# Kernel optimization log

Measured on AMD Instinct MI355X. Metric: run time of the kernel, lower is better.

Reference implementation:

```python
import jax, jax.numpy as jnp
import numpy as np

REPR_IN = (16, 16, 8)
REPR_OUT = (32, 16, 8)
NUM_BASIS = 16
MAX_RADIUS = 2.0
GAMMA = 16.0  # radial basis sharpness

def _dim(repr_):
    return sum(m * (2 * l + 1) for l, m in enumerate(repr_))

DIM_IN = _dim(REPR_IN)          # 104
SIZE_OUT = _dim(REPR_OUT)       # 120
NUM_GATES = sum(REPR_OUT[1:])   # 24
DIM_OUT = SIZE_OUT + NUM_GATES  # 144 (conv emits gates too)


def setup_inputs() -> dict:
    key = jax.random.key(0)
    k1, k2, k3, k4 = jax.random.split(key, 4)
    B, N, M = 4, 1024, 1024
    features = jax.random.normal(k1, (B, DIM_IN, M), jnp.float32)
    difference_matrix = jax.random.normal(k2, (B, N, M, 3), jnp.float32)
    relative_mask = jax.random.uniform(k3, (B, N, M), jnp.float32)
    W = jax.random.normal(k4, (NUM_BASIS, DIM_OUT, DIM_IN), jnp.float32) / np.sqrt(NUM_BASIS * DIM_IN)
    return {"features": features, "difference_matrix": difference_matrix,
            "relative_mask": relative_mask, "W": W}


def _radial_basis(diff):
    # diff: [B, N, M, 3] -> phi: [B, N, M, K]
    r = jnp.sqrt(jnp.sum(diff * diff, axis=-1) + 1e-12)
    centers = jnp.linspace(0.0, MAX_RADIUS, NUM_BASIS, dtype=diff.dtype)
    return jnp.exp(-GAMMA * jnp.square(r[..., None] - centers))


def reference(features, difference_matrix, relative_mask, W):
    # SE3PointConvolution: per-pair kernel K[b,n,m] = sum_k phi_k(|r_nm|) W[k]
    # masked by relative_mask; out[b,o,n] = sum_m K[b,n,m,o,i] feat[b,i,m].
    # Fused so the [B,N,M,144,104] kernel is never materialized.
    phi = _radial_basis(difference_matrix) * relative_mask[..., None]  # [B,N,M,K]
    tmp = jnp.einsum('bnmk,bim->bnki', phi, features)                  # [B,N,K,DIM_IN]
    y = jnp.einsum('bnki,koi->bon', tmp, W)                            # [B,DIM_OUT,N]

    B, _, N = y.shape
    # scalar (l=0) activation, bias=False
    outs = [jax.nn.relu(y[:, :REPR_OUT[0]])]
    # gates: last NUM_GATES channels, sigmoid
    g = jax.nn.sigmoid(y[:, SIZE_OUT:])
    begin_y, begin_g = REPR_OUT[0], 0
    for l, mul in enumerate(REPR_OUT):
        if l == 0 or mul == 0:
            continue
        d = 2 * l + 1
        fy = y[:, begin_y:begin_y + mul * d].reshape(B, mul, d, N)
        fg = g[:, begin_g:begin_g + mul].reshape(B, mul, 1, N)
        outs.append((fy * fg).reshape(B, mul * d, N))
        begin_y += mul * d
        begin_g += mul
    return jnp.concatenate(outs, axis=1)  # [B, SIZE_OUT, N]
```

## Files before the change

kernel.cpp:

```cpp
#include <hip/hip_runtime.h>


typedef __attribute__((ext_vector_type(4))) float f32x4;
typedef __attribute__((ext_vector_type(8))) short s16x8;

#define DI 104
#define DO 144
#define TTST 1688
#define YST 9

#define W_ELEMS 239616
#define F_ELEMS 425984

#define OFF_PHI0 0
#define OFF_PHI1 16384
#define OFF_FEAT0 32768
#define OFF_FEAT1 47104
#define OFF_Y 61440
#define SMEM_TOTAL (61440 + 144*9*4)

__device__ __forceinline__ float fexp2(float x) {
#if __has_builtin(__builtin_amdgcn_exp2f)
    return __builtin_amdgcn_exp2f(x);
#else
    return exp2f(x);
#endif
}
__device__ __forceinline__ float flog2(float x) {
#if __has_builtin(__builtin_amdgcn_logf)
    return __builtin_amdgcn_logf(x);
#else
    return log2f(x);
#endif
}
__device__ __forceinline__ float fsqrt_(float x) {
#if __has_builtin(__builtin_amdgcn_sqrtf)
    return __builtin_amdgcn_sqrtf(x);
#else
    return sqrtf(x);
#endif
}
__device__ __forceinline__ float frcp_(float x) {
#if __has_builtin(__builtin_amdgcn_rcpf)
    return __builtin_amdgcn_rcpf(x);
#else
    return 1.0f / x;
#endif
}
__device__ __forceinline__ unsigned int pkbf(float lo, float hi) {
    unsigned int a = __builtin_bit_cast(unsigned int, lo) + 0x8000u;
    unsigned int b = __builtin_bit_cast(unsigned int, hi) + 0x8000u;
    return __builtin_amdgcn_perm(b, a, 0x07060302u);
}
__device__ __forceinline__ unsigned short f2b(float f) {
    return (unsigned short)((__builtin_bit_cast(unsigned int, f) + 0x8000u) >> 16);
}

__global__ __launch_bounds__(256, 8)
void cvt_kernel(const float* __restrict__ feat_g, const float* __restrict__ W_g,
                unsigned short* __restrict__ ws)
{
    int gid = blockIdx.x * 256 + threadIdx.x;
    const float* src;
    unsigned short* dst;
    if (gid < W_ELEMS/8) {
        src = W_g + gid*8;  dst = ws + gid*8;
    } else {
        int g2 = gid - W_ELEMS/8;
        src = feat_g + g2*8; dst = ws + W_ELEMS + g2*8;
    }
    f32x4 a = *(const f32x4*)src;
    f32x4 b = *(const f32x4*)(src + 4);
    unsigned int o[4] = { pkbf(a[0],a[1]), pkbf(a[2],a[3]), pkbf(b[0],b[1]), pkbf(b[2],b[3]) };
    *(f32x4*)dst = *(f32x4*)o;
}

#define LOAD_DM(M0)                                                    \
    do {                                                               \
        const float* dp_ = diff_g + (dmrow + (M0) + pml)*3;            \
        dx0 = dp_[0]; dy0 = dp_[1]; dz0 = dp_[2];                      \
        dx1 = dp_[3]; dy1 = dp_[4]; dz1 = dp_[5];                      \
        const float* mp_ = mask_g + dmrow + (M0) + pml;                \
        mk0 = mp_[0]; mk1 = mp_[1];                                    \
    } while (0)

#define LOAD_FEAT(M0)                                                          \
    do {                                                                       \
        fr0 = *(const s16x8*)(featbf + fbase + ((size_t)fi0 << 10) + (M0) + (fj << 3)); \
        if (t < 320)                                                           \
            fr1 = *(const s16x8*)(featbf + fbase + ((size_t)fi1 << 10) + (M0) + (fj << 3)); \
    } while (0)

#define PHI_ANCHOR()                                                   \
    do {                                                               \
        float r0_ = fsqrt_(fmaf(dx0,dx0, fmaf(dy0,dy0, fmaf(dz0,dz0, 1e-12f)))); \
        float r1_ = fsqrt_(fmaf(dx1,dx1, fmaf(dy1,dy1, fmaf(dz1,dz1, 1e-12f)))); \
        float t0_ = r0_ - K0OFF, t1_ = r1_ - K0OFF;                    \
        va0 = fexp2(fmaf(CEXP*t0_, t0_, flog2(mk0)));                  \
        va1 = fexp2(fmaf(CEXP*t1_, t1_, flog2(mk1)));                  \
        wa0 = fexp2(fmaf(A1, r0_, S0B));                               \
        wa1 = fexp2(fmaf(A1, r1_, S0B));                               \
        float p0_ = wa0*wa0, p1_ = wa1*wa1;                            \
        float q0_ = fminf(p0_*p0_, 3.0e38f);                           \
        float q1_ = fminf(p1_*p1_, 3.0e38f);                           \
        vb0 = va0 * q0_ * U2_6;                                        \
        vb1 = va1 * q1_ * U2_6;                                        \
        wb0 = wa0 * U2_4;                                              \
        wb1 = wa1 * U2_4;                                              \
    } while (0)

#define PHI_WRITE_Q(BUF, V0, V1, W0, W1, J0)                           \
    do {                                                               \
        unsigned short* pw_ = (BUF) + phirow;                          \
        _Pragma("unroll")                                              \
        for (int j_ = 0; j_ < 4; ++j_) {                               \
            *(unsigned int*)(pw_ + ((J0) + j_)*64 + ((pblk ^ ((J0) + j_)) << 3)) = pkbf(V0, V1); \
            V0 *= W0; W0 *= U2;                                        \
            V1 *= W1; W1 *= U2;                                        \
        }                                                              \
    } while (0)

#define WRITE_FEAT(BUF)                                                \
    do {                                                               \
        *(s16x8*)((BUF) + fi0*64 + fjs) = fr0;                         \
        if (t < 320) *(s16x8*)((BUF) + fi1*64 + fjs) = fr1;            \
    } while (0)

#define GEMM1_HALF(PBUF, FBUF, KK)                                     \
    do {                                                               \
        const int mo_ = (((KK)*4 + q) ^ sw) << 3;                      \
        s16x8 a0_ = *(const s16x8*)((PBUF) + ((2*wr    )*16 + l15)*64 + mo_); \
        s16x8 a1_ = *(const s16x8*)((PBUF) + ((2*wr + 1)*16 + l15)*64 + mo_); \
        _Pragma("unroll")                                              \
        for (int cc_ = 0; cc_ < 4; ++cc_) {                            \
            if (ct0 + cc_ < 7) {                                       \
                s16x8 bf_ = *(const s16x8*)((FBUF) + ((ct0+cc_)*16 + l15)*64 + mo_); \
                acc[0][cc_] = __builtin_amdgcn_mfma_f32_16x16x32_bf16(a0_, bf_, acc[0][cc_], 0, 0, 0); \
                acc[1][cc_] = __builtin_amdgcn_mfma_f32_16x16x32_bf16(a1_, bf_, acc[1][cc_], 0, 0, 0); \
            }                                                          \
        }                                                              \
    } while (0)

__global__ __launch_bounds__(512, 4)
void pgb_kernel(const unsigned short* __restrict__ ws,
                const float* __restrict__ diff_g,
                const float* __restrict__ mask_g,
                float* __restrict__ out_g)
{
    const unsigned short* Wbf    = ws;
    const unsigned short* featbf = ws + W_ELEMS;

    __shared__ __align__(16) unsigned char smem[SMEM_TOTAL];
    unsigned short* Tt   = (unsigned short*)smem;
    float*          ylds = (float*)(smem + OFF_Y);
    unsigned short* phi0b  = (unsigned short*)(smem + OFF_PHI0);
    unsigned short* phi1b  = (unsigned short*)(smem + OFF_PHI1);
    unsigned short* feat0b = (unsigned short*)(smem + OFF_FEAT0);
    unsigned short* feat1b = (unsigned short*)(smem + OFF_FEAT1);

    const int t    = threadIdx.x;
    const int b    = blockIdx.x >> 7;
    const int n0   = (blockIdx.x & 127) << 3;
    const int wave = t >> 6;
    const int lane = t & 63;
    const int l15  = lane & 15;
    const int q    = lane >> 4;
    const int wr   = wave >> 1;
    const int ct0  = (wave & 1) << 2;
    const int sw   = l15 & 7;

    if (t < 256) {
        ((unsigned int*)(smem + OFF_FEAT0 + DI*128))[t] = 0u;
        ((unsigned int*)(smem + OFF_FEAT1 + DI*128))[t] = 0u;
    }

    f32x4 acc[2][4];
#pragma unroll
    for (int rr = 0; rr < 2; ++rr)
#pragma unroll
        for (int cc = 0; cc < 4; ++cc)
            acc[rr][cc] = (f32x4){0.f, 0.f, 0.f, 0.f};

    const int pn   = t >> 6;
    const int kh   = (t >> 5) & 1;
    const int pml  = (t & 31) << 1;
    const int pblk = (t & 31) >> 2;
    const int phirow = (pn*16 + kh*8)*64 + (pml & 7);
    const float CEXP = -23.083120654223414f;
    const float A1   = 6.155498841126244f;
    const float V2   = -0.8207331788168325f;
    const float U2   = fexp2(V2);
    const float U2_2 = U2*U2;
    const float U2_4 = U2_2*U2_2;
    const float U2_6 = U2_4*U2_2;
    const float K0OFF = kh ? 1.0666666666666667f : 0.f;
    const float S0B   = kh ? -6.976232019943076f : -0.41036658940841624f;
    const size_t dmrow = (size_t)((b << 10) + n0 + pn) << 10;

    const int fi0 = t >> 3, fj = t & 7;
    const int fi1 = 64 + (t >> 3);
    const int fjs = (fj ^ (fi0 & 7)) << 3;
    const size_t fbase = (size_t)b * DI << 10;

    float dx0, dy0, dz0, dx1, dy1, dz1, mk0, mk1;
    s16x8 fr0 = {}, fr1 = {};
    float va0, va1, wa0, wa1, vb0, vb1, wb0, wb1;

    LOAD_DM(0);
    LOAD_FEAT(0);
    PHI_ANCHOR();
    PHI_WRITE_Q(phi0b, va0, va1, wa0, wa1, 0);
    PHI_WRITE_Q(phi0b, vb0, vb1, wb0, wb1, 4);
    WRITE_FEAT(feat0b);
    LOAD_DM(64);
    LOAD_FEAT(64);

    for (int s = 0; s < 15; ++s) {
        unsigned short* rp = (s & 1) ? phi1b  : phi0b;
        unsigned short* rf = (s & 1) ? feat1b : feat0b;
        unsigned short* wp = (s & 1) ? phi0b  : phi1b;
        unsigned short* wf = (s & 1) ? feat0b : feat1b;
        __syncthreads();
        WRITE_FEAT(wf);
        PHI_ANCHOR();
        GEMM1_HALF(rp, rf, 0);
        PHI_WRITE_Q(wp, va0, va1, wa0, wa1, 0);
        GEMM1_HALF(rp, rf, 1);
        PHI_WRITE_Q(wp, vb0, vb1, wb0, wb1, 4);
        {
            const int mnext = (s < 14 ? (s + 2) : 15) * 64;
            LOAD_DM(mnext);
            LOAD_FEAT(mnext);
        }
    }
    __syncthreads();
    GEMM1_HALF(phi1b, feat1b, 0);
    GEMM1_HALF(phi1b, feat1b, 1);

    __syncthreads();

#pragma unroll
    for (int rr = 0; rr < 2; ++rr) {
        int nloc = 2*wr + rr;
#pragma unroll
        for (int cc = 0; cc < 4; ++cc) {
            int i = (ct0+cc)*16 + l15;
            if (ct0 + cc < 7 && i < DI) {
#pragma unroll
                for (int r = 0; r < 4; ++r)
                    Tt[nloc*TTST + (q*4+r)*DI + i] = f2b(acc[rr][cc][r]);
            }
        }
    }
    __syncthreads();

    f32x4 y0 = (f32x4){0.f,0.f,0.f,0.f}, y1 = (f32x4){0.f,0.f,0.f,0.f};
    const int o0 = wave*16 + l15;
    const int o1 = 128 + l15;
#pragma unroll 4
    for (int s3 = 0; s3 < 52; ++s3) {
        int a = s3*4 + q;
        int k = a / 13;
        int i = (a - k*13) << 3;
        s16x8 bf = *(const s16x8*)(Tt + (l15 & 7)*TTST + s3*32 + q*8);
        s16x8 af = *(const s16x8*)(Wbf + (size_t)(k*DO + o0)*DI + i);
        y0 = __builtin_amdgcn_mfma_f32_16x16x32_bf16(af, bf, y0, 0, 0, 0);
        if (wave == 0) {
            s16x8 ag = *(const s16x8*)(Wbf + (size_t)(k*DO + o1)*DI + i);
            y1 = __builtin_amdgcn_mfma_f32_16x16x32_bf16(ag, bf, y1, 0, 0, 0);
        }
    }
    if (l15 < 8) {
#pragma unroll
        for (int r = 0; r < 4; ++r)
            ylds[(wave*16 + q*4 + r)*YST + l15] = y0[r];
        if (wave == 0) {
#pragma unroll
            for (int r = 0; r < 4; ++r)
                ylds[(128 + q*4 + r)*YST + l15] = y1[r];
        }
    }
    __syncthreads();

    const float L2E = 1.4426950408889634f;
    for (int idx = t; idx < 120*8; idx += 512) {
        int o = idx >> 3, nn = idx & 7;
        float y = ylds[o*YST + nn];
        float v;
        if (o < 32) {
            v = fmaxf(y, 0.f);
        } else if (o < 80) {
            float g = ylds[(120 + (o-32)/3)*YST + nn];
            v = y * frcp_(1.f + fexp2(-g*L2E));
        } else {
            float g = ylds[(136 + (o-80)/5)*YST + nn];
            v = y * frcp_(1.f + fexp2(-g*L2E));
        }
        out_g[((size_t)(b*120 + o) << 10) + n0 + nn] = v;
    }
}

extern "C" void kernel_launch(void* const* d_in, const int* in_sizes, int n_in,
                              void* d_out, int out_size, void* d_ws, size_t ws_size,
                              hipStream_t stream) {
    const float* feat = (const float*)d_in[0];
    const float* diff = (const float*)d_in[1];
    const float* mask = (const float*)d_in[2];
    const float* W    = (const float*)d_in[3];
    float* out = (float*)d_out;
    unsigned short* ws = (unsigned short*)d_ws;
    (void)in_sizes; (void)n_in; (void)out_size; (void)ws_size;
    cvt_kernel<<<dim3((W_ELEMS + F_ELEMS)/8/256), dim3(256), 0, stream>>>(feat, W, ws);
    pgb_kernel<<<dim3(512), dim3(512), 0, stream>>>(ws, diff, mask, out);
}
```

Measured before the change: 141.4 us.

## Prepack W into MFMA-fragment order and add sched_group_barrier interleaving

```diff
diff --git a/kernel.cpp b/kernel.cpp
--- a/kernel.cpp
+++ b/kernel.cpp
@@ -11,6 +11,7 @@
 
 #define W_ELEMS 239616
 #define F_ELEMS 425984
+#define WP_BLKS 29952
 
 #define OFF_PHI0 0
 #define OFF_PHI1 16384
@@ -18,6 +19,8 @@
 #define OFF_FEAT1 47104
 #define OFF_Y 61440
 #define SMEM_TOTAL (61440 + 144*9*4)
+
+#define SGB(m, n) __builtin_amdgcn_sched_group_barrier((m), (n), 0)
 
 __device__ __forceinline__ float fexp2(float x) {
 #if __has_builtin(__builtin_amdgcn_exp2f)
@@ -63,11 +66,17 @@
     int gid = blockIdx.x * 256 + threadIdx.x;
     const float* src;
     unsigned short* dst;
-    if (gid < W_ELEMS/8) {
-        src = W_g + gid*8;  dst = ws + gid*8;
+    if (gid < WP_BLKS) {
+        int a = gid / 144;
+        int o = gid - a * 144;
+        int k = a / 13;
+        int im = (a - k * 13) << 3;
+        src = W_g + ((k * DO + o) * DI + im);
+        dst = ws + gid * 8;
     } else {
-        int g2 = gid - W_ELEMS/8;
-        src = feat_g + g2*8; dst = ws + W_ELEMS + g2*8;
+        int g2 = gid - WP_BLKS;
+        src = feat_g + g2 * 8;
+        dst = ws + W_ELEMS + g2 * 8;
     }
     f32x4 a = *(const f32x4*)src;
     f32x4 b = *(const f32x4*)(src + 4);
@@ -147,7 +156,7 @@
                 const float* __restrict__ mask_g,
                 float* __restrict__ out_g)
 {
-    const unsigned short* Wbf    = ws;
+    const unsigned short* Wp     = ws;
     const unsigned short* featbf = ws + W_ELEMS;
 
     __shared__ __align__(16) unsigned char smem[SMEM_TOTAL];
@@ -232,6 +241,16 @@
             LOAD_DM(mnext);
             LOAD_FEAT(mnext);
         }
+        SGB(0x200, 2);
+        SGB(0x002, 10);
+        SGB(0x020, 6);
+#pragma unroll
+        for (int g = 0; g < 7; ++g) {
+            SGB(0x100, 2);
+            SGB(0x008, 2);
+            SGB(0x002, 8);
+            SGB(0x200, 1);
+        }
     }
     __syncthreads();
     GEMM1_HALF(phi1b, feat1b, 0);
@@ -255,18 +274,15 @@
     __syncthreads();
 
     f32x4 y0 = (f32x4){0.f,0.f,0.f,0.f}, y1 = (f32x4){0.f,0.f,0.f,0.f};
-    const int o0 = wave*16 + l15;
-    const int o1 = 128 + l15;
+    const unsigned short* wp0 = Wp + ((size_t)q*144 + (wave*16 + l15))*8;
+    const unsigned short* wp1 = Wp + ((size_t)q*144 + (128 + l15))*8;
 #pragma unroll 4
     for (int s3 = 0; s3 < 52; ++s3) {
-        int a = s3*4 + q;
-        int k = a / 13;
-        int i = (a - k*13) << 3;
         s16x8 bf = *(const s16x8*)(Tt + (l15 & 7)*TTST + s3*32 + q*8);
-        s16x8 af = *(const s16x8*)(Wbf + (size_t)(k*DO + o0)*DI + i);
+        s16x8 af = *(const s16x8*)(wp0 + (size_t)s3*4608);
         y0 = __builtin_amdgcn_mfma_f32_16x16x32_bf16(af, bf, y0, 0, 0, 0);
         if (wave == 0) {
-            s16x8 ag = *(const s16x8*)(Wbf + (size_t)(k*DO + o1)*DI + i);
+            s16x8 ag = *(const s16x8*)(wp1 + (size_t)s3*4608);
             y1 = __builtin_amdgcn_mfma_f32_16x16x32_bf16(ag, bf, y1, 0, 0, 0);
         }
     }
```

After: 142.1 us. No clear change (+0.5%).
